# Performance work log

Measured on AMD Instinct MI355X. Metric: run time of the kernel, lower is better.

## Reference

```python
import jax, jax.numpy as jnp
import numpy as np

B, L, D_IN, D_H, N_CLS = 512, 256, 300, 96, 20
N = B * L            # total nodes = 131072
DEG = 8
E = N * DEG          # 1,048,576 edges
VOCAB = 50001        # num_words + 1 (padding row)
STEP = 2
NEG_SLOPE = 0.2


def setup_inputs() -> dict:
    key = jax.random.key(0)
    ks = jax.random.split(key, 24)
    node_ids = jax.random.randint(ks[0], (N,), 0, 50000)
    # block-local edges: each edge stays within its graph's node range
    gid = jnp.repeat(jnp.arange(B), L * DEG)           # [E]
    src = gid * L + jax.random.randint(ks[1], (E,), 0, L)
    dst = gid * L + jax.random.randint(ks[2], (E,), 0, L)

    def xavier(k, shape):
        fan_in, fan_out = shape[0], shape[-1]
        a = float(np.sqrt(6.0 / (fan_in + fan_out)))
        return jax.random.uniform(k, shape, jnp.float32, -a, a)

    inp = {
        "node_ids": node_ids, "src": src, "dst": dst,
        "embed": jax.random.normal(ks[3], (VOCAB, D_IN), jnp.float32),
        "We": xavier(ks[4], (D_IN, D_H)), "be": jnp.zeros((D_H,), jnp.float32),
        "Wg": xavier(ks[5], (D_H, D_H)),
        "att_src": xavier(ks[6], (D_H,)), "att_dst": xavier(ks[7], (D_H,)),
        "bg": jnp.zeros((D_H,), jnp.float32),
        "Wz0": xavier(ks[8], (D_H, D_H)), "bz0": jnp.zeros((D_H,), jnp.float32),
        "Wz1": xavier(ks[9], (D_H, D_H)), "bz1": jnp.zeros((D_H,), jnp.float32),
        "Wr0": xavier(ks[10], (D_H, D_H)), "br0": jnp.zeros((D_H,), jnp.float32),
        "Wr1": xavier(ks[11], (D_H, D_H)), "br1": jnp.zeros((D_H,), jnp.float32),
        "Wh0": xavier(ks[12], (D_H, D_H)), "bh0": jnp.zeros((D_H,), jnp.float32),
        "Wh1": xavier(ks[13], (D_H, D_H)), "bh1": jnp.zeros((D_H,), jnp.float32),
        "Wemb": xavier(ks[14], (D_H, D_H)),
        "Wmlp": xavier(ks[15], (D_H, N_CLS)),
    }
    return inp


def _forward(node_ids, src, dst, embed, We, be, Wg, att_src, att_dst, bg,
             Wz0, bz0, Wz1, bz1, Wr0, br0, Wr1, br1, Wh0, bh0, Wh1, bh1,
             Wemb, Wmlp):
    # embedding lookup + encode (dropout off, eval)
    x = embed[node_ids]                                  # [N, D_IN]
    x = jnp.tanh(x @ We + be)                            # [N, D_H]

    # self loops (GATConv add_self_loops=True, heads=1)
    loop = jnp.arange(N)
    s = jnp.concatenate([src, loop])
    d = jnp.concatenate([dst, loop])

    for _ in range(STEP):
        # ---- GATConv ----
        h = x @ Wg                                       # [N, D_H]
        a_s = h @ att_src                                # [N]
        a_d = h @ att_dst                                # [N]
        e = a_s[s] + a_d[d]
        e = jnp.where(e > 0, e, NEG_SLOPE * e)           # leaky_relu
        # segment softmax over incoming edges of each target node
        m = jax.ops.segment_max(e, d, num_segments=N)
        ex = jnp.exp(e - m[d])
        denom = jax.ops.segment_sum(ex, d, num_segments=N)
        alpha = ex / denom[d]                            # [E+N]
        a = jax.ops.segment_sum(alpha[:, None] * h[s], d, num_segments=N) + bg
        # ---- GRU update (act=tanh) ----
        z = jax.nn.sigmoid(a @ Wz0 + bz0 + x @ Wz1 + bz1)
        r = jax.nn.sigmoid(a @ Wr0 + br0 + x @ Wr1 + br1)
        hh = jnp.tanh(a @ Wh0 + bh0 + (x * r) @ Wh1 + bh1)
        x = hh * z + x * (1.0 - z)

    # graph2batch: equal-length graphs -> reshape, mask is all ones
    xb = x.reshape(B, L, D_H)
    y = jnp.tanh(xb @ Wemb)                              # [B, L, D_H]
    pooled = y.max(axis=1) + y.mean(axis=1)              # max + mean readout
    return pooled @ Wmlp                                 # [B, N_CLS]


def reference(node_ids, src, dst, embed, We, be, Wg, att_src, att_dst, bg,
              Wz0, bz0, Wz1, bz1, Wr0, br0, Wr1, br1, Wh0, bh0, Wh1, bh1,
              Wemb, Wmlp):
    return _forward(node_ids, src, dst, embed, We, be, Wg, att_src, att_dst, bg,
                    Wz0, bz0, Wz1, bz1, Wr0, br0, Wr1, br1, Wh0, bh0, Wh1, bh1,
                    Wemb, Wmlp)
```

## Files before the change

### kernel.cpp

```cpp
#include <hip/hip_runtime.h>
#include <hip/hip_bf16.h>

#define NNODES 131072
#define LGRAPH 256
#define BGRAPH 512
#define DIN 300
#define DH 96
#define EPG 2048
#define VOCAB 50001
#define NCLS 20
#define NEG 0.2f
#define EMB_ROWS 50048
#define EMB_K 320
#define WS 100
#define XS 104

typedef __attribute__((ext_vector_type(4))) float f32x4;
typedef __attribute__((ext_vector_type(8))) short bf16x8;
typedef __attribute__((ext_vector_type(8))) unsigned short u16x8;
#define MFMA16(a, b, c) __builtin_amdgcn_mfma_f32_16x16x32_bf16(a, b, c, 0, 0, 0)

__device__ __forceinline__ unsigned short f2b(float f) {
  __hip_bfloat16 h = __float2bfloat16(f);
  return *reinterpret_cast<unsigned short*>(&h);
}
__device__ __forceinline__ float b2f(unsigned short u) {
  unsigned v = ((unsigned)u) << 16;
  return __uint_as_float(v);
}
__device__ __forceinline__ float sigm(float v) { return 1.f / (1.f + __expf(-v)); }
__device__ __forceinline__ float ftanh(float x) {
  float ax = fabsf(x);
  float e = __expf(ax + ax);
  float t = 1.f - 2.f / (e + 1.f);
  return copysignf(t, x);
}

__global__ void k_prep_w(const float* __restrict__ Wg, const float* __restrict__ Wz0,
                         const float* __restrict__ Wz1, const float* __restrict__ Wr0,
                         const float* __restrict__ Wr1, const float* __restrict__ Wh0,
                         const float* __restrict__ Wh1, const float* __restrict__ Wemb,
                         const float* __restrict__ We,
                         const float* __restrict__ bz0, const float* __restrict__ bz1,
                         const float* __restrict__ br0, const float* __restrict__ br1,
                         const float* __restrict__ bh0, const float* __restrict__ bh1,
                         unsigned short* __restrict__ WT, unsigned short* __restrict__ WeT,
                         float* __restrict__ bc) {
  const int b = blockIdx.x, t = threadIdx.x;
  if (b < 8) {
    const float* src = (b == 0) ? Wg : (b == 1) ? Wz0 : (b == 2) ? Wz1 : (b == 3) ? Wr0
                     : (b == 4) ? Wr1 : (b == 5) ? Wh0 : (b == 6) ? Wh1 : Wemb;
    unsigned short* dst = WT + b * DH * DH;
    for (int i = t; i < DH * DH; i += 256) {
      int c = i / DH, k = i - c * DH;
      dst[i] = f2b(src[k * DH + c]);
    }
  } else if (b == 8) {
    for (int i = t; i < DH * EMB_K; i += 256) {
      int c = i / EMB_K, k = i - c * EMB_K;
      WeT[i] = (k < DIN) ? f2b(We[k * DH + c]) : (unsigned short)0;
    }
  } else {
    if (t < DH) {
      bc[t] = bz0[t] + bz1[t];
      bc[DH + t] = br0[t] + br1[t];
      bc[2 * DH + t] = bh0[t] + bh1[t];
    }
  }
}

__device__ __forceinline__ bf16x8 ldcvt(const float* __restrict__ p, int row, int ko) {
  bf16x8 r;
  if (row < VOCAB) {
    float4 c0 = (ko + 4 <= DIN) ? *(const float4*)&p[row * DIN + ko]
                                : make_float4(0.f, 0.f, 0.f, 0.f);
    float4 c1 = (ko + 8 <= DIN) ? *(const float4*)&p[row * DIN + ko + 4]
                                : make_float4(0.f, 0.f, 0.f, 0.f);
    r[0] = (short)f2b(c0.x); r[1] = (short)f2b(c0.y);
    r[2] = (short)f2b(c0.z); r[3] = (short)f2b(c0.w);
    r[4] = (short)f2b(c1.x); r[5] = (short)f2b(c1.y);
    r[6] = (short)f2b(c1.z); r[7] = (short)f2b(c1.w);
  } else {
    #pragma unroll
    for (int j = 0; j < 8; ++j) r[j] = 0;
  }
  return r;
}

__global__ void k_emb_mm(const float* __restrict__ embed,
                         const unsigned short* __restrict__ WeT,
                         unsigned short* __restrict__ Tb) {
  const int t = threadIdx.x, w = t >> 6, l = t & 63, li = l & 15, lh = l >> 4;
  const int wbase = blockIdx.x * 128 + w * 32;
  f32x4 acc[2][6];
  #pragma unroll
  for (int rt = 0; rt < 2; rt++)
    #pragma unroll
    for (int ct = 0; ct < 6; ct++) acc[rt][ct] = (f32x4)0.f;
  for (int ks = 0; ks < 10; ++ks) {
    const int ko = lh * 8 + ks * 32;
    bf16x8 aA0 = ldcvt(embed, wbase + li, ko);
    bf16x8 aA1 = ldcvt(embed, wbase + 16 + li, ko);
    #pragma unroll
    for (int ct = 0; ct < 6; ct++) {
      bf16x8 bB = *(const bf16x8*)&WeT[(ct * 16 + li) * EMB_K + ko];
      acc[0][ct] = MFMA16(aA0, bB, acc[0][ct]);
      acc[1][ct] = MFMA16(aA1, bB, acc[1][ct]);
    }
  }
  #pragma unroll
  for (int rt = 0; rt < 2; rt++)
    #pragma unroll
    for (int ct = 0; ct < 6; ct++)
      #pragma unroll
      for (int r = 0; r < 4; r++)
        Tb[(wbase + rt * 16 + lh * 4 + r) * DH + ct * 16 + li] = f2b(acc[rt][ct][r]);
}

__global__ __launch_bounds__(256) void k_gh(
    const int* __restrict__ ids, const unsigned short* __restrict__ Tb,
    const float* __restrict__ be, const unsigned short* __restrict__ WgT,
    const float* __restrict__ att_s, const float* __restrict__ att_d,
    unsigned short* __restrict__ xb, unsigned short* __restrict__ h,
    float* __restrict__ a_s, float* __restrict__ a_d) {
  __shared__ __align__(16) unsigned short sX[128 * XS];
  __shared__ int s_id[128];
  __shared__ float s_be[DH];
  const int t = threadIdx.x, w = t >> 6, l = t & 63, li = l & 15, lh = l >> 4;
  const int nb0 = blockIdx.x * 128;
  bf16x8 WF[6][3];
  #pragma unroll
  for (int ct = 0; ct < 6; ++ct)
    #pragma unroll
    for (int ks = 0; ks < 3; ++ks)
      WF[ct][ks] = *(const bf16x8*)&WgT[(ct * 16 + li) * DH + lh * 8 + ks * 32];
  if (t < 128) s_id[t] = ids[nb0 + t];
  if (t < DH) s_be[t] = be[t];
  __syncthreads();
  #pragma unroll
  for (int j = 0; j < 6; ++j) {
    int idx = t + 256 * j;
    int row = idx / 12, ch = idx - row * 12;
    u16x8 v = *(const u16x8*)&Tb[s_id[row] * DH + ch * 8];
    u16x8 o;
    #pragma unroll
    for (int k = 0; k < 8; ++k) o[k] = f2b(ftanh(b2f(v[k]) + s_be[ch * 8 + k]));
    *(u16x8*)&sX[row * XS + ch * 8] = o;
    *(u16x8*)&xb[(nb0 + row) * DH + ch * 8] = o;
  }
  __syncthreads();
  const int wbase = w * 32;
  f32x4 acc[2][6];
  #pragma unroll
  for (int rt = 0; rt < 2; rt++)
    #pragma unroll
    for (int ct = 0; ct < 6; ct++) acc[rt][ct] = (f32x4)0.f;
  bf16x8 aA[2][3];
  #pragma unroll
  for (int rt = 0; rt < 2; rt++)
    #pragma unroll
    for (int ks = 0; ks < 3; ks++)
      aA[rt][ks] = *(const bf16x8*)&sX[(wbase + rt * 16 + li) * XS + lh * 8 + ks * 32];
  #pragma unroll
  for (int ks = 0; ks < 3; ++ks)
    #pragma unroll
    for (int ct = 0; ct < 6; ct++) {
      acc[0][ct] = MFMA16(aA[0][ks], WF[ct][ks], acc[0][ct]);
      acc[1][ct] = MFMA16(aA[1][ks], WF[ct][ks], acc[1][ct]);
    }
  float ps[2][4] = {}, pd[2][4] = {};
  #pragma unroll
  for (int rt = 0; rt < 2; rt++)
    #pragma unroll
    for (int ct = 0; ct < 6; ct++) {
      const int col = ct * 16 + li;
      const float as_ = att_s[col], ad_ = att_d[col];
      #pragma unroll
      for (int r = 0; r < 4; r++) {
        float v = acc[rt][ct][r];
        h[(nb0 + wbase + rt * 16 + lh * 4 + r) * DH + col] = f2b(v);
        ps[rt][r] += v * as_;
        pd[rt][r] += v * ad_;
      }
    }
  #pragma unroll
  for (int rt = 0; rt < 2; rt++)
    #pragma unroll
    for (int r = 0; r < 4; r++) {
      float s = ps[rt][r], d = pd[rt][r];
      #pragma unroll
      for (int m = 1; m < 16; m <<= 1) { s += __shfl_xor(s, m); d += __shfl_xor(d, m); }
      if (li == 0) {
        const int row = nb0 + wbase + rt * 16 + lh * 4 + r;
        a_s[row] = s;
        a_d[row] = d;
      }
    }
}

__global__ __launch_bounds__(256) void k_h(
    const unsigned short* __restrict__ xb, const unsigned short* __restrict__ WgT,
    const float* __restrict__ att_s, const float* __restrict__ att_d,
    unsigned short* __restrict__ h, float* __restrict__ a_s,
    float* __restrict__ a_d) {
  __shared__ __align__(16) unsigned short sW[DH * WS];
  const int t = threadIdx.x, w = t >> 6, l = t & 63, li = l & 15, lh = l >> 4;
  const int wbase = blockIdx.x * 128 + w * 32;
  for (int i = t; i < DH * 12; i += 256) {
    int r = i / 12, c8 = i - r * 12;
    *(int4*)&sW[r * WS + c8 * 8] = *(const int4*)&WgT[r * DH + c8 * 8];
  }
  __syncthreads();
  f32x4 acc[2][6];
  #pragma unroll
  for (int rt = 0; rt < 2; rt++)
    #pragma unroll
    for (int ct = 0; ct < 6; ct++) acc[rt][ct] = (f32x4)0.f;
  #pragma unroll
  for (int ks = 0; ks < 3; ++ks) {
    const int ko = lh * 8 + ks * 32;
    bf16x8 aA0 = *(const bf16x8*)&xb[(wbase + li) * DH + ko];
    bf16x8 aA1 = *(const bf16x8*)&xb[(wbase + 16 + li) * DH + ko];
    #pragma unroll
    for (int ct = 0; ct < 6; ct++) {
      bf16x8 bB = *(const bf16x8*)&sW[(ct * 16 + li) * WS + ko];
      acc[0][ct] = MFMA16(aA0, bB, acc[0][ct]);
      acc[1][ct] = MFMA16(aA1, bB, acc[1][ct]);
    }
  }
  float ps[2][4] = {}, pd[2][4] = {};
  #pragma unroll
  for (int rt = 0; rt < 2; rt++)
    #pragma unroll
    for (int ct = 0; ct < 6; ct++) {
      const int col = ct * 16 + li;
      const float as_ = att_s[col], ad_ = att_d[col];
      #pragma unroll
      for (int r = 0; r < 4; r++) {
        float v = acc[rt][ct][r];
        h[(wbase + rt * 16 + lh * 4 + r) * DH + col] = f2b(v);
        ps[rt][r] += v * as_;
        pd[rt][r] += v * ad_;
      }
    }
  #pragma unroll
  for (int rt = 0; rt < 2; rt++)
    #pragma unroll
    for (int r = 0; r < 4; r++) {
      float s = ps[rt][r], d = pd[rt][r];
      #pragma unroll
      for (int m = 1; m < 16; m <<= 1) { s += __shfl_xor(s, m); d += __shfl_xor(d, m); }
      if (li == 0) {
        const int row = wbase + rt * 16 + lh * 4 + r;
        a_s[row] = s;
        a_d[row] = d;
      }
    }
}

__global__ __launch_bounds__(1024, 8) void k_att(
    const int* __restrict__ src, const int* __restrict__ dst,
    const unsigned short* __restrict__ h, const float* __restrict__ a_sg,
    const float* __restrict__ a_dg, const float* __restrict__ bg,
    unsigned short* __restrict__ aout) {
  __shared__ __align__(16) unsigned short sH[LGRAPH * XS];
  __shared__ float s_ev[EPG];
  __shared__ unsigned char s_sl[EPG], s_dl[EPG];
  __shared__ unsigned char s_srcS[EPG];
  __shared__ int s_cnt[LGRAPH], s_off[LGRAPH], s_pos[LGRAPH];
  __shared__ float s_as[LGRAPH], s_ad[LGRAPH];
  __shared__ float s_bg[DH];
  const int g = blockIdx.x, t = threadIdx.x;
  const int nb = g * LGRAPH;
  if (t < LGRAPH) { s_cnt[t] = 0; s_as[t] = a_sg[nb + t]; s_ad[t] = a_dg[nb + t]; }
  if (t < DH) s_bg[t] = bg[t];
  #pragma unroll
  for (int j = 0; j < 3; ++j) {
    int idx = t + 1024 * j;
    int row = idx / 12, ch = idx - row * 12;
    *(int4*)&sH[row * XS + ch * 8] = *(const int4*)&h[(nb + row) * DH + ch * 8];
  }
  __syncthreads();
  for (int e = t; e < EPG; e += 1024) {
    int sl = src[g * EPG + e] - nb, dl = dst[g * EPG + e] - nb;
    s_sl[e] = (unsigned char)sl;
    s_dl[e] = (unsigned char)dl;
    atomicAdd(&s_cnt[dl], 1);
  }
  __syncthreads();
  if (t < 64) {
    int carry = 0;
    #pragma unroll
    for (int c = 0; c < 4; ++c) {
      int v = s_cnt[c * 64 + t];
      int x = v;
      #pragma unroll
      for (int o = 1; o < 64; o <<= 1) {
        int y = __shfl_up(x, o);
        if (t >= o) x += y;
      }
      s_off[c * 64 + t] = x - v + carry;
      carry += __shfl(x, 63);
    }
  }
  __syncthreads();
  if (t < LGRAPH) s_pos[t] = s_off[t];
  __syncthreads();
  for (int e = t; e < EPG; e += 1024) {
    int sl = s_sl[e], dl = s_dl[e];
    float ee = s_as[sl] + s_ad[dl];
    ee = ee > 0.f ? ee : NEG * ee;
    int pos = atomicAdd(&s_pos[dl], 1);
    s_srcS[pos] = (unsigned char)sl;
    s_ev[pos] = ee;
  }
  __syncthreads();
  {
    const int d = t >> 2;
    const int cbase = (t & 3) * 24;
    const int beg = s_off[d], end = beg + s_cnt[d];
    float ss = s_as[d] + s_ad[d];
    ss = ss > 0.f ? ss : NEG * ss;
    float m = ss;
    for (int i = beg; i < end; ++i) m = fmaxf(m, s_ev[i]);
    float acc[24];
    float wself = __expf(ss - m);
    float den = wself;
    #pragma unroll
    for (int k = 0; k < 3; ++k) {
      u16x8 v = *(const u16x8*)&sH[d * XS + cbase + k * 8];
      #pragma unroll
      for (int j = 0; j < 8; ++j) acc[k * 8 + j] = wself * b2f(v[j]);
    }
    for (int i = beg; i < end; ++i) {
      float wv = __expf(s_ev[i] - m);
      den += wv;
      int sl2 = s_srcS[i];
      #pragma unroll
      for (int k = 0; k < 3; ++k) {
        u16x8 v = *(const u16x8*)&sH[sl2 * XS + cbase + k * 8];
        #pragma unroll
        for (int j = 0; j < 8; ++j) acc[k * 8 + j] += wv * b2f(v[j]);
      }
    }
    float inv = 1.f / den;
    unsigned short* op = &aout[(nb + d) * DH + cbase];
    #pragma unroll
    for (int k = 0; k < 3; ++k) {
      u16x8 o;
      #pragma unroll
      for (int j = 0; j < 8; ++j) o[j] = f2b(acc[k * 8 + j] * inv + s_bg[cbase + k * 8 + j]);
      *(u16x8*)&op[k * 8] = o;
    }
  }
}

__global__ __launch_bounds__(1024, 4) void k_gru(
    const unsigned short* __restrict__ ab, unsigned short* __restrict__ xb,
    const unsigned short* __restrict__ WT, const float* __restrict__ bc) {
  __shared__ __align__(16) unsigned short sW[6 * DH * WS];
  __shared__ __align__(16) unsigned short sX[128 * WS];
  const int t = threadIdx.x, w = t >> 6, l = t & 63, li = l & 15, lh = l >> 4;
  const int wr = w >> 1, wc = w & 1;
  #pragma unroll
  for (int m = 0; m < 6; ++m) {
    const int srcm = (m == 0) ? 3 : (m == 1) ? 4 : (m == 2) ? 1 : (m == 3) ? 2 : (m == 4) ? 5 : 6;
    const unsigned short* srcp = WT + srcm * DH * DH;
    for (int i = t; i < DH * 12; i += 1024) {
      int r = i / 12, c8 = i - r * 12;
      *(int4*)&sW[(m * DH + r) * WS + c8 * 8] = *(const int4*)&srcp[r * DH + c8 * 8];
    }
  }
  float zb_[3], rb_[3], hb_[3];
  #pragma unroll
  for (int ct = 0; ct < 3; ++ct) {
    const int col = wc * 48 + ct * 16 + li;
    zb_[ct] = bc[col]; rb_[ct] = bc[DH + col]; hb_[ct] = bc[2 * DH + col];
  }

  for (int tile = 0; tile < 4; ++tile) {
    const int nb0 = (blockIdx.x * 4 + tile) * 128;
    __syncthreads();
    for (int idx = t; idx < 1536; idx += 1024) {
      int row = idx / 12, ch = idx - row * 12;
      *(int4*)&sX[row * WS + ch * 8] = *(const int4*)&xb[(nb0 + row) * DH + ch * 8];
    }
    __syncthreads();
    bf16x8 aA[3], aX[3];
    #pragma unroll
    for (int ks = 0; ks < 3; ks++) {
      const int row = wr * 16 + li;
      const int ko = lh * 8 + ks * 32;
      aA[ks] = *(const bf16x8*)&ab[(nb0 + row) * DH + ko];
      aX[ks] = *(const bf16x8*)&sX[row * WS + ko];
    }
    float xo[3][4];
    #pragma unroll
    for (int ct = 0; ct < 3; ct++)
      #pragma unroll
      for (int r = 0; r < 4; r++)
        xo[ct][r] = b2f(sX[(wr * 16 + lh * 4 + r) * WS + wc * 48 + ct * 16 + li]);
    f32x4 accR[3], accZ[3];
    #pragma unroll
    for (int ct = 0; ct < 3; ct++) { accR[ct] = (f32x4)0.f; accZ[ct] = (f32x4)0.f; }
    #pragma unroll
    for (int ks = 0; ks < 3; ks++) {
      const int ko = lh * 8 + ks * 32;
      #pragma unroll
      for (int ct = 0; ct < 3; ct++) {
        const int wrow = wc * 48 + ct * 16 + li;
        bf16x8 w_r0 = *(const bf16x8*)&sW[(0 * DH + wrow) * WS + ko];
        bf16x8 w_r1 = *(const bf16x8*)&sW[(1 * DH + wrow) * WS + ko];
        bf16x8 w_z0 = *(const bf16x8*)&sW[(2 * DH + wrow) * WS + ko];
        bf16x8 w_z1 = *(const bf16x8*)&sW[(3 * DH + wrow) * WS + ko];
        accR[ct] = MFMA16(aA[ks], w_r0, accR[ct]);
        accR[ct] = MFMA16(aX[ks], w_r1, accR[ct]);
        accZ[ct] = MFMA16(aA[ks], w_z0, accZ[ct]);
        accZ[ct] = MFMA16(aX[ks], w_z1, accZ[ct]);
      }
    }
    __syncthreads();
    #pragma unroll
    for (int ct = 0; ct < 3; ct++) {
      const int col = wc * 48 + ct * 16 + li;
      #pragma unroll
      for (int r = 0; r < 4; r++) {
        float rv = sigm(accR[ct][r] + rb_[ct]);
        sX[(wr * 16 + lh * 4 + r) * WS + col] = f2b(xo[ct][r] * rv);
      }
    }
    __syncthreads();
    bf16x8 aU[3];
    #pragma unroll
    for (int ks = 0; ks < 3; ks++)
      aU[ks] = *(const bf16x8*)&sX[(wr * 16 + li) * WS + lh * 8 + ks * 32];
    __syncthreads();
    f32x4 accH[3];
    #pragma unroll
    for (int ct = 0; ct < 3; ct++) accH[ct] = (f32x4)0.f;
    #pragma unroll
    for (int ks = 0; ks < 3; ks++) {
      const int ko = lh * 8 + ks * 32;
      #pragma unroll
      for (int ct = 0; ct < 3; ct++) {
        const int wrow = wc * 48 + ct * 16 + li;
        bf16x8 w_h0 = *(const bf16x8*)&sW[(4 * DH + wrow) * WS + ko];
        bf16x8 w_h1 = *(const bf16x8*)&sW[(5 * DH + wrow) * WS + ko];
        accH[ct] = MFMA16(aA[ks], w_h0, accH[ct]);
        accH[ct] = MFMA16(aU[ks], w_h1, accH[ct]);
      }
    }
    #pragma unroll
    for (int ct = 0; ct < 3; ct++) {
      const int col = wc * 48 + ct * 16 + li;
      #pragma unroll
      for (int r = 0; r < 4; r++) {
        float z = sigm(accZ[ct][r] + zb_[ct]);
        float hh = ftanh(accH[ct][r] + hb_[ct]);
        float xn = hh * z + xo[ct][r] * (1.f - z);
        sX[(wr * 16 + lh * 4 + r) * WS + col] = f2b(xn);
      }
    }
    __syncthreads();
    for (int idx = t; idx < 1536; idx += 1024) {
      int row = idx / 12, ch = idx - row * 12;
      *(int4*)&xb[(nb0 + row) * DH + ch * 8] = *(const int4*)&sX[row * WS + ch * 8];
    }
  }
}

__global__ __launch_bounds__(256) void k_readout(
    const unsigned short* __restrict__ xb, const unsigned short* __restrict__ WembT,
    const float* __restrict__ Wmlp, float* __restrict__ out) {
  __shared__ __align__(16) unsigned short sW[DH * WS];
  __shared__ float pmaxs[4][DH], psums[4][DH];
  __shared__ float spool[DH];
  const int g = blockIdx.x, t = threadIdx.x, w = t >> 6, l = t & 63, li = l & 15, lh = l >> 4;
  const int wbase = g * LGRAPH + w * 64;
  for (int i = t; i < DH * 12; i += 256) {
    int r = i / 12, c8 = i - r * 12;
    *(int4*)&sW[r * WS + c8 * 8] = *(const int4*)&WembT[r * DH + c8 * 8];
  }
  __syncthreads();
  f32x4 acc[4][6];
  #pragma unroll
  for (int rt = 0; rt < 4; rt++)
    #pragma unroll
    for (int ct = 0; ct < 6; ct++) acc[rt][ct] = (f32x4)0.f;
  #pragma unroll
  for (int ks = 0; ks < 3; ks++) {
    const int ko = lh * 8 + ks * 32;
    bf16x8 aA[4];
    #pragma unroll
    for (int rt = 0; rt < 4; rt++)
      aA[rt] = *(const bf16x8*)&xb[(wbase + rt * 16 + li) * DH + ko];
    #pragma unroll
    for (int ct = 0; ct < 6; ct++) {
      bf16x8 bB = *(const bf16x8*)&sW[(ct * 16 + li) * WS + ko];
      #pragma unroll
      for (int rt = 0; rt < 4; rt++) acc[rt][ct] = MFMA16(aA[rt], bB, acc[rt][ct]);
    }
  }
  float pm[6], psu[6];
  #pragma unroll
  for (int ct = 0; ct < 6; ct++) {
    float mx = -1e30f, sm = 0.f;
    #pragma unroll
    for (int rt = 0; rt < 4; rt++)
      #pragma unroll
      for (int r = 0; r < 4; r++) {
        float y = ftanh(acc[rt][ct][r]);
        mx = fmaxf(mx, y);
        sm += y;
      }
    pm[ct] = mx; psu[ct] = sm;
  }
  #pragma unroll
  for (int ct = 0; ct < 6; ct++) {
    pm[ct] = fmaxf(pm[ct], __shfl_xor(pm[ct], 16));
    psu[ct] += __shfl_xor(psu[ct], 16);
    pm[ct] = fmaxf(pm[ct], __shfl_xor(pm[ct], 32));
    psu[ct] += __shfl_xor(psu[ct], 32);
  }
  if (lh == 0) {
    #pragma unroll
    for (int ct = 0; ct < 6; ct++) {
      pmaxs[w][ct * 16 + li] = pm[ct];
      psums[w][ct * 16 + li] = psu[ct];
    }
  }
  __syncthreads();
  if (t < DH) {
    float mx = fmaxf(fmaxf(pmaxs[0][t], pmaxs[1][t]), fmaxf(pmaxs[2][t], pmaxs[3][t]));
    float sm = psums[0][t] + psums[1][t] + psums[2][t] + psums[3][t];
    spool[t] = mx + sm * (1.f / LGRAPH);
  }
  __syncthreads();
  if (t < NCLS) {
    float a = 0.f;
    for (int k = 0; k < DH; ++k) a += spool[k] * Wmlp[k * NCLS + t];
    out[g * NCLS + t] = a;
  }
}

extern "C" void kernel_launch(void* const* d_in, const int* in_sizes, int n_in,
                              void* d_out, int out_size, void* d_ws, size_t ws_size,
                              hipStream_t stream) {
  const int*   node_ids = (const int*)d_in[0];
  const int*   src      = (const int*)d_in[1];
  const int*   dst      = (const int*)d_in[2];
  const float* embed    = (const float*)d_in[3];
  const float* We   = (const float*)d_in[4];
  const float* be   = (const float*)d_in[5];
  const float* Wg   = (const float*)d_in[6];
  const float* att_src = (const float*)d_in[7];
  const float* att_dst = (const float*)d_in[8];
  const float* bg   = (const float*)d_in[9];
  const float* Wz0  = (const float*)d_in[10];
  const float* bz0  = (const float*)d_in[11];
  const float* Wz1  = (const float*)d_in[12];
  const float* bz1  = (const float*)d_in[13];
  const float* Wr0  = (const float*)d_in[14];
  const float* br0  = (const float*)d_in[15];
  const float* Wr1  = (const float*)d_in[16];
  const float* br1  = (const float*)d_in[17];
  const float* Wh0  = (const float*)d_in[18];
  const float* bh0  = (const float*)d_in[19];
  const float* Wh1  = (const float*)d_in[20];
  const float* bh1  = (const float*)d_in[21];
  const float* Wemb = (const float*)d_in[22];
  const float* Wmlp = (const float*)d_in[23];
  float* out = (float*)d_out;

  char* w_ = (char*)d_ws;
  unsigned short* xb   = (unsigned short*)(w_ + 0);
  unsigned short* ab   = (unsigned short*)(w_ + 25165824);
  unsigned short* h    = (unsigned short*)(w_ + 50331648);
  unsigned short* Tb   = (unsigned short*)(w_ + 75497472);
  float*          a_s  = (float*)(w_ + 85106688);
  float*          a_d  = (float*)(w_ + 85630976);
  unsigned short* WT   = (unsigned short*)(w_ + 86155264);
  unsigned short* WeT  = (unsigned short*)(w_ + 86302720);
  float*          bc   = (float*)(w_ + 86364160);

  unsigned short* WgT   = WT + 0 * DH * DH;
  unsigned short* WembT = WT + 7 * DH * DH;

  hipLaunchKernelGGL(k_prep_w, dim3(10), dim3(256), 0, stream,
                     Wg, Wz0, Wz1, Wr0, Wr1, Wh0, Wh1, Wemb, We,
                     bz0, bz1, br0, br1, bh0, bh1, WT, WeT, bc);
  hipLaunchKernelGGL(k_emb_mm, dim3(EMB_ROWS / 128), dim3(256), 0, stream, embed, WeT, Tb);
  hipLaunchKernelGGL(k_gh, dim3(NNODES / 128), dim3(256), 0, stream,
                     node_ids, Tb, be, WgT, att_src, att_dst, xb, h, a_s, a_d);
  hipLaunchKernelGGL(k_att, dim3(BGRAPH), dim3(1024), 0, stream,
                     src, dst, h, a_s, a_d, bg, ab);
  hipLaunchKernelGGL(k_gru, dim3(256), dim3(1024), 0, stream, ab, xb, WT, bc);
  hipLaunchKernelGGL(k_h, dim3(NNODES / 128), dim3(256), 0, stream,
                     xb, WgT, att_src, att_dst, h, a_s, a_d);
  hipLaunchKernelGGL(k_att, dim3(BGRAPH), dim3(1024), 0, stream,
                     src, dst, h, a_s, a_d, bg, ab);
  hipLaunchKernelGGL(k_gru, dim3(256), dim3(1024), 0, stream, ab, xb, WT, bc);
  hipLaunchKernelGGL(k_readout, dim3(BGRAPH), dim3(256), 0, stream, xb, WembT, Wmlp, out);
}
```

Before: 239.4 us.

## Give each GRU wave full rows to remove block-wide barriers

The GRU kernel now runs 512 threads (8 waves), and each wave owns 16 full rows across all 96 output columns instead of half the columns. Each wave loads and stores only its own rows of x in shared memory, so all per-tile __syncthreads barriers are removed and only wave-local dependencies remain. The cost is twice the accumulators and weight reads per wave, which raises register pressure, and half the threads per block.

```diff
diff --git a/kernel.cpp b/kernel.cpp
--- a/kernel.cpp
+++ b/kernel.cpp
@@ -355,60 +355,61 @@
   }
 }
 
-__global__ __launch_bounds__(1024, 4) void k_gru(
+__global__ __launch_bounds__(512, 2) void k_gru(
     const unsigned short* __restrict__ ab, unsigned short* __restrict__ xb,
     const unsigned short* __restrict__ WT, const float* __restrict__ bc) {
   __shared__ __align__(16) unsigned short sW[6 * DH * WS];
   __shared__ __align__(16) unsigned short sX[128 * WS];
   const int t = threadIdx.x, w = t >> 6, l = t & 63, li = l & 15, lh = l >> 4;
-  const int wr = w >> 1, wc = w & 1;
   #pragma unroll
   for (int m = 0; m < 6; ++m) {
     const int srcm = (m == 0) ? 3 : (m == 1) ? 4 : (m == 2) ? 1 : (m == 3) ? 2 : (m == 4) ? 5 : 6;
     const unsigned short* srcp = WT + srcm * DH * DH;
-    for (int i = t; i < DH * 12; i += 1024) {
+    for (int i = t; i < DH * 12; i += 512) {
       int r = i / 12, c8 = i - r * 12;
       *(int4*)&sW[(m * DH + r) * WS + c8 * 8] = *(const int4*)&srcp[r * DH + c8 * 8];
     }
   }
-  float zb_[3], rb_[3], hb_[3];
-  #pragma unroll
-  for (int ct = 0; ct < 3; ++ct) {
-    const int col = wc * 48 + ct * 16 + li;
+  float zb_[6], rb_[6], hb_[6];
+  #pragma unroll
+  for (int ct = 0; ct < 6; ++ct) {
+    const int col = ct * 16 + li;
     zb_[ct] = bc[col]; rb_[ct] = bc[DH + col]; hb_[ct] = bc[2 * DH + col];
   }
+  __syncthreads();
+  const int r0 = w * 16;
 
   for (int tile = 0; tile < 4; ++tile) {
     const int nb0 = (blockIdx.x * 4 + tile) * 128;
-    __syncthreads();
-    for (int idx = t; idx < 1536; idx += 1024) {
-      int row = idx / 12, ch = idx - row * 12;
-      *(int4*)&sX[row * WS + ch * 8] = *(const int4*)&xb[(nb0 + row) * DH + ch * 8];
-    }
-    __syncthreads();
+    #pragma unroll
+    for (int j = 0; j < 3; ++j) {
+      int idx = l + 64 * j;
+      int rr = idx / 12, ch = idx - rr * 12;
+      *(int4*)&sX[(r0 + rr) * WS + ch * 8] =
+          *(const int4*)&xb[(nb0 + r0 + rr) * DH + ch * 8];
+    }
     bf16x8 aA[3], aX[3];
-    #pragma unroll
-    for (int ks = 0; ks < 3; ks++) {
-      const int row = wr * 16 + li;
-      const int ko = lh * 8 + ks * 32;
-      aA[ks] = *(const bf16x8*)&ab[(nb0 + row) * DH + ko];
-      aX[ks] = *(const bf16x8*)&sX[row * WS + ko];
-    }
-    float xo[3][4];
-    #pragma unroll
-    for (int ct = 0; ct < 3; ct++)
-      #pragma unroll
-      for (int r = 0; r < 4; r++)
-        xo[ct][r] = b2f(sX[(wr * 16 + lh * 4 + r) * WS + wc * 48 + ct * 16 + li]);
-    f32x4 accR[3], accZ[3];
-    #pragma unroll
-    for (int ct = 0; ct < 3; ct++) { accR[ct] = (f32x4)0.f; accZ[ct] = (f32x4)0.f; }
     #pragma unroll
     for (int ks = 0; ks < 3; ks++) {
       const int ko = lh * 8 + ks * 32;
-      #pragma unroll
-      for (int ct = 0; ct < 3; ct++) {
-        const int wrow = wc * 48 + ct * 16 + li;
+      aA[ks] = *(const bf16x8*)&ab[(nb0 + r0 + li) * DH + ko];
+      aX[ks] = *(const bf16x8*)&sX[(r0 + li) * WS + ko];
+    }
+    float xo[6][4];
+    #pragma unroll
+    for (int ct = 0; ct < 6; ct++)
+      #pragma unroll
+      for (int r = 0; r < 4; r++)
+        xo[ct][r] = b2f(sX[(r0 + lh * 4 + r) * WS + ct * 16 + li]);
+    f32x4 accR[6], accZ[6];
+    #pragma unroll
+    for (int ct = 0; ct < 6; ct++) { accR[ct] = (f32x4)0.f; accZ[ct] = (f32x4)0.f; }
+    #pragma unroll
+    for (int ks = 0; ks < 3; ks++) {
+      const int ko = lh * 8 + ks * 32;
+      #pragma unroll
+      for (int ct = 0; ct < 6; ct++) {
+        const int wrow = ct * 16 + li;
         bf16x8 w_r0 = *(const bf16x8*)&sW[(0 * DH + wrow) * WS + ko];
         bf16x8 w_r1 = *(const bf16x8*)&sW[(1 * DH + wrow) * WS + ko];
         bf16x8 w_z0 = *(const bf16x8*)&sW[(2 * DH + wrow) * WS + ko];
@@ -419,31 +420,28 @@
         accZ[ct] = MFMA16(aX[ks], w_z1, accZ[ct]);
       }
     }
-    __syncthreads();
-    #pragma unroll
-    for (int ct = 0; ct < 3; ct++) {
-      const int col = wc * 48 + ct * 16 + li;
+    #pragma unroll
+    for (int ct = 0; ct < 6; ct++) {
+      const int col = ct * 16 + li;
       #pragma unroll
       for (int r = 0; r < 4; r++) {
         float rv = sigm(accR[ct][r] + rb_[ct]);
-        sX[(wr * 16 + lh * 4 + r) * WS + col] = f2b(xo[ct][r] * rv);
-      }
-    }
-    __syncthreads();
+        sX[(r0 + lh * 4 + r) * WS + col] = f2b(xo[ct][r] * rv);
+      }
+    }
     bf16x8 aU[3];
     #pragma unroll
     for (int ks = 0; ks < 3; ks++)
-      aU[ks] = *(const bf16x8*)&sX[(wr * 16 + li) * WS + lh * 8 + ks * 32];
-    __syncthreads();
-    f32x4 accH[3];
-    #pragma unroll
-    for (int ct = 0; ct < 3; ct++) accH[ct] = (f32x4)0.f;
+      aU[ks] = *(const bf16x8*)&sX[(r0 + li) * WS + lh * 8 + ks * 32];
+    f32x4 accH[6];
+    #pragma unroll
+    for (int ct = 0; ct < 6; ct++) accH[ct] = (f32x4)0.f;
     #pragma unroll
     for (int ks = 0; ks < 3; ks++) {
       const int ko = lh * 8 + ks * 32;
       #pragma unroll
-      for (int ct = 0; ct < 3; ct++) {
-        const int wrow = wc * 48 + ct * 16 + li;
+      for (int ct = 0; ct < 6; ct++) {
+        const int wrow = ct * 16 + li;
         bf16x8 w_h0 = *(const bf16x8*)&sW[(4 * DH + wrow) * WS + ko];
         bf16x8 w_h1 = *(const bf16x8*)&sW[(5 * DH + wrow) * WS + ko];
         accH[ct] = MFMA16(aA[ks], w_h0, accH[ct]);
@@ -451,20 +449,22 @@
       }
     }
     #pragma unroll
-    for (int ct = 0; ct < 3; ct++) {
-      const int col = wc * 48 + ct * 16 + li;
+    for (int ct = 0; ct < 6; ct++) {
+      const int col = ct * 16 + li;
       #pragma unroll
       for (int r = 0; r < 4; r++) {
         float z = sigm(accZ[ct][r] + zb_[ct]);
         float hh = ftanh(accH[ct][r] + hb_[ct]);
         float xn = hh * z + xo[ct][r] * (1.f - z);
-        sX[(wr * 16 + lh * 4 + r) * WS + col] = f2b(xn);
-      }
-    }
-    __syncthreads();
-    for (int idx = t; idx < 1536; idx += 1024) {
-      int row = idx / 12, ch = idx - row * 12;
-      *(int4*)&xb[(nb0 + row) * DH + ch * 8] = *(const int4*)&sX[row * WS + ch * 8];
+        sX[(r0 + lh * 4 + r) * WS + col] = f2b(xn);
+      }
+    }
+    #pragma unroll
+    for (int j = 0; j < 3; ++j) {
+      int idx = l + 64 * j;
+      int rr = idx / 12, ch = idx - rr * 12;
+      *(int4*)&xb[(nb0 + r0 + rr) * DH + ch * 8] =
+          *(const int4*)&sX[(r0 + rr) * WS + ch * 8];
     }
   }
 }
@@ -594,11 +594,11 @@
                      node_ids, Tb, be, WgT, att_src, att_dst, xb, h, a_s, a_d);
   hipLaunchKernelGGL(k_att, dim3(BGRAPH), dim3(1024), 0, stream,
                      src, dst, h, a_s, a_d, bg, ab);
-  hipLaunchKernelGGL(k_gru, dim3(256), dim3(1024), 0, stream, ab, xb, WT, bc);
+  hipLaunchKernelGGL(k_gru, dim3(256), dim3(512), 0, stream, ab, xb, WT, bc);
   hipLaunchKernelGGL(k_h, dim3(NNODES / 128), dim3(256), 0, stream,
                      xb, WgT, att_src, att_dst, h, a_s, a_d);
   hipLaunchKernelGGL(k_att, dim3(BGRAPH), dim3(1024), 0, stream,
                      src, dst, h, a_s, a_d, bg, ab);
-  hipLaunchKernelGGL(k_gru, dim3(256), dim3(1024), 0, stream, ab, xb, WT, bc);
+  hipLaunchKernelGGL(k_gru, dim3(256), dim3(512), 0, stream, ab, xb, WT, bc);
   hipLaunchKernelGGL(k_readout, dim3(BGRAPH), dim3(256), 0, stream, xb, WembT, Wmlp, out);
 }
```

After: 475.0 us. +98.4%, slower.
